# Optimization experiments

Measured on AMD Instinct MI355X. Metric: run time of the kernel, lower is better.

The kernel has to match this reference:

```python
import jax, jax.numpy as jnp
import numpy as np

GAMMA = 0.001
B, D = 8192, 128


def setup_inputs() -> dict:
    key = jax.random.key(0)
    inputs = jax.random.normal(key, (B, D), dtype=jnp.float32)
    # N-pair style labels: every sample has exactly one same-label partner
    targets = jnp.repeat(jnp.arange(B // 2, dtype=jnp.int32), 2)
    return {"inputs": inputs, "targets": targets}


def reference(inputs, targets):
    b = inputs.shape[0]
    # [B,B] scaled similarity matrix
    W = GAMMA * (inputs @ inputs.T)
    same = targets[:, None] == targets[None, :]
    offdiag = ~jnp.eye(b, dtype=bool)
    # first other index with the same label (original takes the first match)
    pos_idx = jnp.argmax(same & offdiag, axis=1)            # [B]
    Wpos = jnp.take_along_axis(W, pos_idx[:, None], axis=1)  # [B,1]
    # negatives = everything except the query itself and its positive
    neg_mask = offdiag.at[jnp.arange(b), pos_idx].set(False)
    s = jnp.sum(jnp.exp(W - Wpos) * neg_mask, axis=1)        # [B]
    return jnp.mean(jnp.log1p(s))
```

## Files before the change

### kernel.cpp

```cpp
#include <hip/hip_runtime.h>
#include <hip/hip_bf16.h>
#include <math.h>

#define GAMMA 0.001f
#define HG2   5.0e-7f
#define Bn 8192
#define Dk 128
#define NGP 256

typedef float f32x4 __attribute__((ext_vector_type(4)));
typedef short bf16x8 __attribute__((ext_vector_type(8)));


__device__ inline ushort f2b(float x) {
    union { __hip_bfloat16 h; ushort u; } c;
    c.h = __float2bfloat16(x);
    return c.u;
}
__device__ inline float b2f(ushort u) { return __uint_as_float(((unsigned)u) << 16); }

__launch_bounds__(512)
__global__ void k_gpart(const float* __restrict__ X, ushort* __restrict__ Xb,
                        ushort* __restrict__ Gpb, float* __restrict__ Sp,
                        unsigned* __restrict__ counter) {
    int bid = blockIdx.x, tid = threadIdx.x;
    __shared__ float xl[32 * 128];
    const float4* src = reinterpret_cast<const float4*>(X) + (size_t)bid * 1024;
    float4* dl = reinterpret_cast<float4*>(xl);
    ushort4* xbo = reinterpret_cast<ushort4*>(Xb) + (size_t)bid * 1024;
#pragma unroll
    for (int it = 0; it < 2; ++it) {
        int idx = tid + it * 512;
        float4 v = src[idx];
        dl[idx] = v;
        ushort4 u;
        u.x = f2b(v.x); u.y = f2b(v.y); u.z = f2b(v.z); u.w = f2b(v.w);
        xbo[idx] = u;
    }
    if (bid == 0 && tid == 0) *counter = 0u;
    __syncthreads();

    int tr = (tid >> 4) * 4, tc = (tid & 15) * 8;
    float acc[4][8];
#pragma unroll
    for (int i = 0; i < 4; ++i)
#pragma unroll
        for (int j = 0; j < 8; ++j) acc[i][j] = 0.f;
#pragma unroll 4
    for (int k = 0; k < 32; ++k) {
        const float* rowk = &xl[k * 128];
        float a[4], b[8];
        *(float4*)&a[0] = *(const float4*)&rowk[tr];
        *(float4*)&b[0] = *(const float4*)&rowk[tc];
        *(float4*)&b[4] = *(const float4*)&rowk[tc + 4];
#pragma unroll
        for (int i = 0; i < 4; ++i)
#pragma unroll
            for (int j = 0; j < 8; ++j) acc[i][j] += a[i] * b[j];
    }
    ushort* gpo = Gpb + (size_t)bid * 16384 + tr * 128 + tc;
#pragma unroll
    for (int i = 0; i < 4; ++i) {
        union { ushort s[8]; uint4 v; } pk;
#pragma unroll
        for (int j = 0; j < 8; ++j) pk.s[j] = f2b(acc[i][j]);
        *reinterpret_cast<uint4*>(gpo + i * 128) = pk.v;
    }
    if (tid < 128) {
        float sc = 0.f;
#pragma unroll
        for (int k = 0; k < 32; ++k) sc += xl[k * 128 + tid];
        Sp[bid * 128 + tid] = sc;
    }
}

__global__ void k_mid(const ushort* __restrict__ Gpb, ushort* __restrict__ Gb,
                      const float* __restrict__ Sp, float* __restrict__ S) {
    int bid = blockIdx.x, tid = threadIdx.x;
    if (bid < 128) {
        int el = tid & 15, pc = tid >> 4;
        int eg = bid * 16 + el;
        float a8[8];
#pragma unroll
        for (int j = 0; j < 8; ++j) a8[j] = 0.f;
        const ushort* base = Gpb + (size_t)eg * 8;
#pragma unroll 4
        for (int k = 0; k < 16; ++k) {
            int p = pc + k * 16;
            union { uint4 v; ushort s[8]; } ld;
            ld.v = *reinterpret_cast<const uint4*>(base + (size_t)p * 16384);
#pragma unroll
            for (int j = 0; j < 8; ++j) a8[j] += b2f(ld.s[j]);
        }
        __shared__ float red[16][16][8];
        __shared__ float red2[128];
#pragma unroll
        for (int j = 0; j < 8; ++j) red[pc][el][j] = a8[j];
        __syncthreads();
        if (tid < 128) {
            int e2 = tid >> 3, j = tid & 7;
            float v = 0.f;
#pragma unroll
            for (int p = 0; p < 16; ++p) v += red[p][e2][j];
            red2[e2 * 8 + j] = v;
        }
        __syncthreads();
        if (tid < 16) {
            union { ushort s[8]; uint4 v; } pk;
#pragma unroll
            for (int j = 0; j < 8; ++j) pk.s[j] = f2b(red2[tid * 8 + j]);
            *reinterpret_cast<uint4*>(Gb + (size_t)(bid * 16 + tid) * 8) = pk.v;
        }
    } else {
        if (tid < 128) {
            float sc = 0.f;
            for (int p = 0; p < NGP; ++p) sc += Sp[p * 128 + tid];
            S[tid] = sc;
        }
    }
}

__device__ inline void prep_pairs(int u, int lane, const float* __restrict__ X,
                                  const int* __restrict__ tgt,
                                  const float* __restrict__ S,
                                  float* __restrict__ em, float* __restrict__ pre) {
    float sv0 = S[lane], sv1 = S[lane + 64];
    for (int pr = u; pr < Bn / 2; pr += 512) {
        int i0 = pr * 2, i1 = i0 + 1;
        float x0 = X[(size_t)i0 * 128 + lane], x1 = X[(size_t)i0 * 128 + 64 + lane];
        float y0 = X[(size_t)i1 * 128 + lane], y1 = X[(size_t)i1 * 128 + 64 + lane];
        float ds0 = x0 * x0 + x1 * x1;
        float ds1 = y0 * y0 + y1 * y1;
        float dp  = x0 * y0 + x1 * y1;
        float sl0 = x0 * sv0 + x1 * sv1;
        float sl1 = y0 * sv0 + y1 * sv1;
        for (int off = 32; off; off >>= 1) {
            ds0 += __shfl_xor(ds0, off);
            ds1 += __shfl_xor(ds1, off);
            dp  += __shfl_xor(dp,  off);
            sl0 += __shfl_xor(sl0, off);
            sl1 += __shfl_xor(sl1, off);
        }
        int t0 = tgt[i0], t1 = tgt[i1];
        if (t0 == t1) {
            if (lane == 0) {
                float wp = GAMMA * dp;
                float e = __expf(-wp);
                float tp = 1.0f + wp + 0.5f * wp * wp;
                float w0 = GAMMA * ds0, w1 = GAMMA * ds1;
                em[i0] = e;
                em[i1] = e;
                pre[i0] = 8192.0f + GAMMA * sl0 - (1.0f + w0 + 0.5f * w0 * w0) - tp;
                pre[i1] = 8192.0f + GAMMA * sl1 - (1.0f + w1 + 0.5f * w1 * w1) - tp;
            }
        } else {
#pragma unroll
            for (int h = 0; h < 2; ++h) {
                int i  = h ? i1 : i0;
                int ti = h ? t1 : t0;
                float a0 = h ? y0 : x0, a1 = h ? y1 : x1;
                float dsi = h ? ds1 : ds0, sli = h ? sl1 : sl0;
                int pos = 0;
                for (int c0 = 0; c0 < Bn; c0 += 64) {
                    int j = c0 + lane;
                    bool m = (tgt[j] == ti) && (j != i);
                    unsigned long long mk = __ballot(m);
                    if (mk) { pos = c0 + __ffsll(mk) - 1; break; }
                }
                float p0 = X[(size_t)pos * 128 + lane], p1 = X[(size_t)pos * 128 + 64 + lane];
                float dpi = a0 * p0 + a1 * p1;
                for (int off = 32; off; off >>= 1) dpi += __shfl_xor(dpi, off);
                if (lane == 0) {
                    float wp = GAMMA * dpi, wi = GAMMA * dsi;
                    em[i] = __expf(-wp);
                    pre[i] = 8192.0f + GAMMA * sli
                             - (1.0f + wi + 0.5f * wi * wi)
                             - (1.0f + wp + 0.5f * wp * wp);
                }
            }
        }
    }
}

__launch_bounds__(256, 2)
__global__ void k_main(const ushort* __restrict__ Xb, const ushort* __restrict__ Gb,
                       const float* __restrict__ X, const int* __restrict__ tgt,
                       const float* __restrict__ S,
                       float* __restrict__ qpart, float* __restrict__ em,
                       float* __restrict__ pre) {
    int bid = blockIdx.x, tid = threadIdx.x;
    int lane = tid & 63, wid = tid >> 6;
    if (bid < 64) {
        __shared__ ushort sm[32768];
        const ushort* gA = Xb + (size_t)bid * 16384;
#pragma unroll
        for (int it = 0; it < 8; ++it) {
            int ob = wid * 512 + it * 64;
            int o = ob + lane;
            int src = (o & ~15) | ((o & 15) ^ ((o >> 4) & 7));
            __builtin_amdgcn_global_load_lds(
                (const __attribute__((address_space(1))) void*)(gA + (size_t)src * 8),
                (__attribute__((address_space(3))) void*)(sm + ob * 8), 16, 0, 0);
            __builtin_amdgcn_global_load_lds(
                (const __attribute__((address_space(1))) void*)(Gb + (size_t)src * 8),
                (__attribute__((address_space(3))) void*)(sm + 16384 + ob * 8), 16, 0, 0);
        }
        __syncthreads();
        int wm = wid >> 1, wn = wid & 1, r15 = lane & 15, khalf = lane >> 4;
        const bf16x8* XA = reinterpret_cast<const bf16x8*>(sm);
        const bf16x8* GBL = reinterpret_cast<const bf16x8*>(sm + 16384);
        f32x4 acc[4][4];
#pragma unroll
        for (int m = 0; m < 4; ++m)
#pragma unroll
            for (int n = 0; n < 4; ++n) acc[m][n] = (f32x4){0.f, 0.f, 0.f, 0.f};
#pragma unroll
        for (int ks = 0; ks < 4; ++ks) {
            int u0 = ks * 4 + khalf;
            bf16x8 a[4], b[4];
#pragma unroll
            for (int m = 0; m < 4; ++m) {
                int row = wm * 64 + m * 16 + r15;
                a[m] = XA[row * 16 + (u0 ^ (row & 7))];
            }
#pragma unroll
            for (int n = 0; n < 4; ++n) {
                int row = wn * 64 + n * 16 + r15;
                b[n] = GBL[row * 16 + (u0 ^ (row & 7))];
            }
#pragma unroll
            for (int m = 0; m < 4; ++m)
#pragma unroll
                for (int n = 0; n < 4; ++n)
                    acc[m][n] = __builtin_amdgcn_mfma_f32_16x16x32_bf16(a[m], b[n], acc[m][n], 0, 0, 0);
        }
        float qp[4][4];
#pragma unroll
        for (int m = 0; m < 4; ++m)
#pragma unroll
            for (int r = 0; r < 4; ++r) qp[m][r] = 0.f;
#pragma unroll
        for (int m = 0; m < 4; ++m)
#pragma unroll
            for (int n = 0; n < 4; ++n) {
                int c = wn * 64 + n * 16 + r15;
#pragma unroll
                for (int r = 0; r < 4; ++r) {
                    int il = wm * 64 + m * 16 + khalf * 4 + r;
                    ushort xu = sm[il * 128 + (((c >> 3) ^ (il & 7)) << 3) + (c & 7)];
                    qp[m][r] += acc[m][n][r] * b2f(xu);
                }
            }
#pragma unroll
        for (int m = 0; m < 4; ++m)
#pragma unroll
            for (int r = 0; r < 4; ++r) {
                float v = qp[m][r];
                v += __shfl_xor(v, 1);
                v += __shfl_xor(v, 2);
                v += __shfl_xor(v, 4);
                v += __shfl_xor(v, 8);
                qp[m][r] = v;
            }
        if (r15 == 0) {
#pragma unroll
            for (int m = 0; m < 4; ++m)
#pragma unroll
                for (int r = 0; r < 4; ++r)
                    qpart[(size_t)wn * Bn + bid * 128 + wm * 64 + m * 16 + khalf * 4 + r] = qp[m][r];
        }
    } else {
        prep_pairs((bid - 64) * 4 + wid, lane, X, tgt, S, em, pre);
    }
}

__global__ void k_fin(const float* __restrict__ qpart, const float* __restrict__ em,
                      const float* __restrict__ pre, float* __restrict__ blocksum,
                      unsigned* __restrict__ counter, float* __restrict__ out) {
    int bid = blockIdx.x, tid = threadIdx.x;
    float v = 0.f;
#pragma unroll
    for (int h = 0; h < 2; ++h) {
        int r = bid * 512 + h * 256 + tid;
        float q = qpart[r] + qpart[Bn + r];
        float s = em[r] * (pre[r] + HG2 * q);
        v += log1pf(s);
    }
    for (int off = 32; off; off >>= 1) v += __shfl_xor(v, off);
    __shared__ float a4[4];
    __shared__ bool last;
    int lane = tid & 63, wid = tid >> 6;
    if (lane == 0) a4[wid] = v;
    __syncthreads();
    if (tid == 0) {
        blocksum[bid] = a4[0] + a4[1] + a4[2] + a4[3];
        __threadfence();
        unsigned old = atomicAdd(counter, 1u);
        last = (old == 15u);
    }
    __syncthreads();
    if (last && tid < 16) {
        __threadfence();
        float x = ((volatile float*)blocksum)[tid];
        x += __shfl_xor(x, 1);
        x += __shfl_xor(x, 2);
        x += __shfl_xor(x, 4);
        x += __shfl_xor(x, 8);
        if (tid == 0) out[0] = x * (1.0f / 8192.0f);
    }
}

extern "C" void kernel_launch(void* const* d_in, const int* in_sizes, int n_in,
                              void* d_out, int out_size, void* d_ws, size_t ws_size,
                              hipStream_t stream) {
    const float* X  = (const float*)d_in[0];
    const int* tgt  = (const int*)d_in[1];
    float* out      = (float*)d_out;
    char* ws        = (char*)d_ws;

    const size_t MB = 1024 * 1024;
    ushort* Xb        = (ushort*)ws;
    ushort* Gpb       = (ushort*)(ws + 2 * MB);
    ushort* Gb        = (ushort*)(ws + 10 * MB);
    float* Sp         = (float*)(ws + 10 * MB + 32 * 1024);
    float* S          = (float*)(ws + 10 * MB + 192 * 1024);
    float* em         = (float*)(ws + 11 * MB);
    float* pre        = (float*)(ws + 11 * MB + 32 * 1024);
    float* qpart      = (float*)(ws + 11 * MB + 64 * 1024);
    float* blocksum   = (float*)(ws + 11 * MB + 128 * 1024);
    unsigned* counter = (unsigned*)(ws + 11 * MB + 128 * 1024 + 256);

    k_gpart<<<NGP, 512, 0, stream>>>(X, Xb, Gpb, Sp, counter);
    k_mid<<<129, 256, 0, stream>>>(Gpb, Gb, Sp, S);
    k_main<<<192, 256, 0, stream>>>(Xb, Gb, X, tgt, S, qpart, em, pre);
    k_fin<<<16, 256, 0, stream>>>(qpart, em, pre, blocksum, counter, out);
}
```

Measured before the change: 31.44 us.

## Halve Gram partials by 64-row chunks split across two blocks

The partial Gram kernel now works on 128 chunks of 64 rows instead of 256 chunks of 32. Each chunk is handled by two blocks that each compute half of the 128x128 output rows, so the number of bf16 partial matrices written and later reduced in k_mid halves. Each block loads 64 rows into shared memory, with 32KB of LDS per block. The pair prep also switches to float2 vectorized loads of X and S. Costs: every chunk of X is read twice and shared-memory use per block doubles.

```diff
diff --git a/kernel.cpp b/kernel.cpp
--- a/kernel.cpp
+++ b/kernel.cpp
@@ -6,7 +6,7 @@
 #define HG2   5.0e-7f
 #define Bn 8192
 #define Dk 128
-#define NGP 256
+#define NCH 128
 
 typedef float f32x4 __attribute__((ext_vector_type(4)));
 typedef short bf16x8 __attribute__((ext_vector_type(8)));
@@ -24,53 +24,57 @@
                         ushort* __restrict__ Gpb, float* __restrict__ Sp,
                         unsigned* __restrict__ counter) {
     int bid = blockIdx.x, tid = threadIdx.x;
-    __shared__ float xl[32 * 128];
-    const float4* src = reinterpret_cast<const float4*>(X) + (size_t)bid * 1024;
+    int chunk = bid & (NCH - 1), half = bid >> 7;
+    __shared__ float xl[64 * 128];
+    const float4* src = reinterpret_cast<const float4*>(X) + (size_t)chunk * 2048;
     float4* dl = reinterpret_cast<float4*>(xl);
-    ushort4* xbo = reinterpret_cast<ushort4*>(Xb) + (size_t)bid * 1024;
-#pragma unroll
-    for (int it = 0; it < 2; ++it) {
+    ushort4* xbo = reinterpret_cast<ushort4*>(Xb) + (size_t)chunk * 2048;
+#pragma unroll
+    for (int it = 0; it < 4; ++it) {
         int idx = tid + it * 512;
         float4 v = src[idx];
         dl[idx] = v;
-        ushort4 u;
-        u.x = f2b(v.x); u.y = f2b(v.y); u.z = f2b(v.z); u.w = f2b(v.w);
-        xbo[idx] = u;
+        if (half == 0) {
+            ushort4 u;
+            u.x = f2b(v.x); u.y = f2b(v.y); u.z = f2b(v.z); u.w = f2b(v.w);
+            xbo[idx] = u;
+        }
     }
     if (bid == 0 && tid == 0) *counter = 0u;
     __syncthreads();
 
-    int tr = (tid >> 4) * 4, tc = (tid & 15) * 8;
-    float acc[4][8];
-#pragma unroll
-    for (int i = 0; i < 4; ++i)
+    int tr = half * 64 + (tid >> 4) * 2, tc = (tid & 15) * 8;
+    float acc[2][8];
+#pragma unroll
+    for (int i = 0; i < 2; ++i)
 #pragma unroll
         for (int j = 0; j < 8; ++j) acc[i][j] = 0.f;
 #pragma unroll 4
-    for (int k = 0; k < 32; ++k) {
+    for (int k = 0; k < 64; ++k) {
         const float* rowk = &xl[k * 128];
-        float a[4], b[8];
-        *(float4*)&a[0] = *(const float4*)&rowk[tr];
+        float a0 = rowk[tr], a1 = rowk[tr + 1];
+        float b[8];
         *(float4*)&b[0] = *(const float4*)&rowk[tc];
         *(float4*)&b[4] = *(const float4*)&rowk[tc + 4];
 #pragma unroll
-        for (int i = 0; i < 4; ++i)
-#pragma unroll
-            for (int j = 0; j < 8; ++j) acc[i][j] += a[i] * b[j];
-    }
-    ushort* gpo = Gpb + (size_t)bid * 16384 + tr * 128 + tc;
-#pragma unroll
-    for (int i = 0; i < 4; ++i) {
+        for (int j = 0; j < 8; ++j) {
+            acc[0][j] += a0 * b[j];
+            acc[1][j] += a1 * b[j];
+        }
+    }
+    ushort* gpo = Gpb + (size_t)chunk * 16384 + tr * 128 + tc;
+#pragma unroll
+    for (int i = 0; i < 2; ++i) {
         union { ushort s[8]; uint4 v; } pk;
 #pragma unroll
         for (int j = 0; j < 8; ++j) pk.s[j] = f2b(acc[i][j]);
         *reinterpret_cast<uint4*>(gpo + i * 128) = pk.v;
     }
-    if (tid < 128) {
+    if (half == 0 && tid < 128) {
         float sc = 0.f;
-#pragma unroll
-        for (int k = 0; k < 32; ++k) sc += xl[k * 128 + tid];
-        Sp[bid * 128 + tid] = sc;
+#pragma unroll 8
+        for (int k = 0; k < 64; ++k) sc += xl[k * 128 + tid];
+        Sp[chunk * 128 + tid] = sc;
     }
 }
 
@@ -84,8 +88,8 @@
 #pragma unroll
         for (int j = 0; j < 8; ++j) a8[j] = 0.f;
         const ushort* base = Gpb + (size_t)eg * 8;
-#pragma unroll 4
-        for (int k = 0; k < 16; ++k) {
+#pragma unroll
+        for (int k = 0; k < 8; ++k) {
             int p = pc + k * 16;
             union { uint4 v; ushort s[8]; } ld;
             ld.v = *reinterpret_cast<const uint4*>(base + (size_t)p * 16384);
@@ -114,7 +118,7 @@
     } else {
         if (tid < 128) {
             float sc = 0.f;
-            for (int p = 0; p < NGP; ++p) sc += Sp[p * 128 + tid];
+            for (int p = 0; p < NCH; ++p) sc += Sp[p * 128 + tid];
             S[tid] = sc;
         }
     }
@@ -124,16 +128,16 @@
                                   const int* __restrict__ tgt,
                                   const float* __restrict__ S,
                                   float* __restrict__ em, float* __restrict__ pre) {
-    float sv0 = S[lane], sv1 = S[lane + 64];
+    float2 sv = *reinterpret_cast<const float2*>(&S[lane * 2]);
     for (int pr = u; pr < Bn / 2; pr += 512) {
         int i0 = pr * 2, i1 = i0 + 1;
-        float x0 = X[(size_t)i0 * 128 + lane], x1 = X[(size_t)i0 * 128 + 64 + lane];
-        float y0 = X[(size_t)i1 * 128 + lane], y1 = X[(size_t)i1 * 128 + 64 + lane];
-        float ds0 = x0 * x0 + x1 * x1;
-        float ds1 = y0 * y0 + y1 * y1;
-        float dp  = x0 * y0 + x1 * y1;
-        float sl0 = x0 * sv0 + x1 * sv1;
-        float sl1 = y0 * sv0 + y1 * sv1;
+        float2 xv = *reinterpret_cast<const float2*>(&X[(size_t)i0 * 128 + lane * 2]);
+        float2 yv = *reinterpret_cast<const float2*>(&X[(size_t)i1 * 128 + lane * 2]);
+        float ds0 = xv.x * xv.x + xv.y * xv.y;
+        float ds1 = yv.x * yv.x + yv.y * yv.y;
+        float dp  = xv.x * yv.x + xv.y * yv.y;
+        float sl0 = xv.x * sv.x + xv.y * sv.y;
+        float sl1 = yv.x * sv.x + yv.y * sv.y;
         for (int off = 32; off; off >>= 1) {
             ds0 += __shfl_xor(ds0, off);
             ds1 += __shfl_xor(ds1, off);
@@ -158,7 +162,7 @@
             for (int h = 0; h < 2; ++h) {
                 int i  = h ? i1 : i0;
                 int ti = h ? t1 : t0;
-                float a0 = h ? y0 : x0, a1 = h ? y1 : x1;
+                float a0 = h ? yv.x : xv.x, a1 = h ? yv.y : xv.y;
                 float dsi = h ? ds1 : ds0, sli = h ? sl1 : sl0;
                 int pos = 0;
                 for (int c0 = 0; c0 < Bn; c0 += 64) {
@@ -167,8 +171,8 @@
                     unsigned long long mk = __ballot(m);
                     if (mk) { pos = c0 + __ffsll(mk) - 1; break; }
                 }
-                float p0 = X[(size_t)pos * 128 + lane], p1 = X[(size_t)pos * 128 + 64 + lane];
-                float dpi = a0 * p0 + a1 * p1;
+                float2 pv = *reinterpret_cast<const float2*>(&X[(size_t)pos * 128 + lane * 2]);
+                float dpi = a0 * pv.x + a1 * pv.y;
                 for (int off = 32; off; off >>= 1) dpi += __shfl_xor(dpi, off);
                 if (lane == 0) {
                     float wp = GAMMA * dpi, wi = GAMMA * dsi;
@@ -330,7 +334,7 @@
     float* blocksum   = (float*)(ws + 11 * MB + 128 * 1024);
     unsigned* counter = (unsigned*)(ws + 11 * MB + 128 * 1024 + 256);
 
-    k_gpart<<<NGP, 512, 0, stream>>>(X, Xb, Gpb, Sp, counter);
+    k_gpart<<<2 * NCH, 512, 0, stream>>>(X, Xb, Gpb, Sp, counter);
     k_mid<<<129, 256, 0, stream>>>(Gpb, Gb, Sp, S);
     k_main<<<192, 256, 0, stream>>>(Xb, Gb, X, tgt, S, qpart, em, pre);
     k_fin<<<16, 256, 0, stream>>>(qpart, em, pre, blocksum, counter, out);
```

Result: faster. 28.30 us (median of 2 runs) (-10.0%).
